# Kernel tuning notes

Hardware: AMD Instinct MI355X
Metric: run time of the kernel (lower is better)

The kernel has to match this reference:

```python
import jax, jax.numpy as jnp
import numpy as np

D_MODEL = 1024
N_HEADS = 16
D_FF = 2 * D_MODEL
EPS = 1e-6


def setup_inputs() -> dict:
    key = jax.random.key(0)
    ks = jax.random.split(key, 12)
    B, S, D = 2, 2048, D_MODEL
    w = lambda k, shape: (jax.random.normal(k, shape, dtype=jnp.float32) * 0.02)
    return {
        "x": jax.random.normal(ks[0], (B, S, D), dtype=jnp.float32),
        "mask": jnp.ones((B, S, S), dtype=jnp.int32),
        "alpha1": jnp.ones((D,), jnp.float32),
        "bias1": jnp.zeros((D,), jnp.float32),
        "Wq": w(ks[1], (D, D)), "bq": jnp.zeros((D,), jnp.float32),
        "Wk": w(ks[2], (D, D)), "bk": jnp.zeros((D,), jnp.float32),
        "Wv": w(ks[3], (D, D)), "bv": jnp.zeros((D,), jnp.float32),
        "Wo": w(ks[4], (D, D)), "bo": jnp.zeros((D,), jnp.float32),
        "alpha2": jnp.ones((D,), jnp.float32),
        "bias2": jnp.zeros((D,), jnp.float32),
        "W1": w(ks[5], (D, D_FF)), "b1": jnp.zeros((D_FF,), jnp.float32),
        "W2": w(ks[6], (D_FF, D)), "b2": jnp.zeros((D,), jnp.float32),
    }


def _norm(x, alpha, bias):
    # torch: alpha*(x-mean)/(std+eps)+bias, std is unbiased (ddof=1)
    mu = jnp.mean(x, axis=-1, keepdims=True)
    sd = jnp.std(x, axis=-1, ddof=1, keepdims=True)
    return alpha * (x - mu) / (sd + EPS) + bias


def _gelu(x):
    return jax.nn.gelu(x, approximate=False)  # torch F.gelu exact


def _attention(x2, mask, Wq, bq, Wk, bk, Wv, bv, Wo, bo):
    B, S, D = x2.shape
    h, dk = N_HEADS, D // N_HEADS
    # project and split heads: [B, h, S, dk]
    q = (x2 @ Wq + bq).reshape(B, S, h, dk).transpose(0, 2, 1, 3)
    k = (x2 @ Wk + bk).reshape(B, S, h, dk).transpose(0, 2, 1, 3)
    v = (x2 @ Wv + bv).reshape(B, S, h, dk).transpose(0, 2, 1, 3)
    scores = jnp.einsum('bhqd,bhkd->bhqk', q, k) / np.sqrt(dk).astype(np.float32)
    scores = jnp.where(mask[:, None] == 0, jnp.float32(-1e9), scores)
    attn = jax.nn.softmax(scores, axis=-1)
    out = jnp.einsum('bhqk,bhkd->bhqd', attn, v)
    out = out.transpose(0, 2, 1, 3).reshape(B, S, D)
    return out @ Wo + bo


def reference(x, mask, alpha1, bias1, Wq, bq, Wk, bk, Wv, bv, Wo, bo,
              alpha2, bias2, W1, b1, W2, b2):
    x2 = _norm(x, alpha1, bias1)
    x = x + _attention(x2, mask, Wq, bq, Wk, bk, Wv, bv, Wo, bo)
    x2 = _norm(x, alpha2, bias2)
    ff = _gelu(_gelu(x2 @ W1 + b1) @ W2 + b2)
    return x + ff
```

## Files before the change

kernel.cpp:

```cpp
#include <hip/hip_runtime.h>
#include <math.h>

typedef __attribute__((ext_vector_type(8))) short v8s;
typedef __attribute__((ext_vector_type(4))) float v4f;
typedef __attribute__((ext_vector_type(16))) float v16f;
typedef __attribute__((ext_vector_type(4))) unsigned int v4u;
typedef __attribute__((ext_vector_type(2))) unsigned int v2u;

#define MFMA16(a,b,c) __builtin_amdgcn_mfma_f32_16x16x32_bf16(a,b,c,0,0,0)
#define MFMA32(a,b,c) __builtin_amdgcn_mfma_f32_32x32x16_bf16(a,b,c,0,0,0)
#define QSCALE 0.18033688011112042f

typedef const __attribute__((address_space(1))) void* gp1_t;
typedef __attribute__((address_space(3))) void* lp3_t;
__device__ __forceinline__ void gll16(const void* g, void* l){
  __builtin_amdgcn_global_load_lds((gp1_t)g, (lp3_t)l, 16, 0, 0);
}
#define VMCNT(n) asm volatile("s_waitcnt vmcnt(" #n ")" ::: "memory")

__device__ __forceinline__ unsigned short f2b(float f){
  unsigned u = __builtin_bit_cast(unsigned, f);
  u += 0x7FFFu + ((u>>16)&1u);
  return (unsigned short)(u>>16);
}
__device__ __forceinline__ unsigned cvtpk(float lo, float hi){
  unsigned r;
  asm("v_cvt_pk_bf16_f32 %0, %1, %2" : "=v"(r) : "v"(lo), "v"(hi));
  return r;
}
__device__ __forceinline__ float gelu_exact(float x){
  return 0.5f*x*(1.0f + erff(x*0.70710678118654752f));
}

__global__ __launch_bounds__(256) void ln_kernel(const float* __restrict__ x,
    const float* __restrict__ alpha, const float* __restrict__ bias,
    unsigned short* __restrict__ out)
{
  const int D = 1024;
  int row = blockIdx.x;
  int tid = threadIdx.x;
  const float* xr = x + (size_t)row*D;
  v4f v = ((const v4f*)xr)[tid];
  float s  = v[0]+v[1]+v[2]+v[3];
  float s2 = v[0]*v[0]+v[1]*v[1]+v[2]*v[2]+v[3]*v[3];
  #pragma unroll
  for (int off=1; off<64; off<<=1){ s += __shfl_xor(s, off); s2 += __shfl_xor(s2, off); }
  __shared__ float red[8];
  int w = tid>>6;
  if ((tid&63)==0){ red[w]=s; red[4+w]=s2; }
  __syncthreads();
  s  = red[0]+red[1]+red[2]+red[3];
  s2 = red[4]+red[5]+red[6]+red[7];
  float mu  = s*(1.0f/D);
  float var = (s2 - (float)D*mu*mu)*(1.0f/(D-1));
  float inv = 1.0f/(sqrtf(fmaxf(var,0.0f)) + 1e-6f);
  v4f a  = ((const v4f*)alpha)[tid];
  v4f bi = ((const v4f*)bias)[tid];
  unsigned short o[4];
  #pragma unroll
  for (int i=0;i<4;i++) o[i] = f2b(a[i]*(v[i]-mu)*inv + bi[i]);
  v2u pk; pk[0] = (unsigned)o[0] | ((unsigned)o[1]<<16);
          pk[1] = (unsigned)o[2] | ((unsigned)o[3]<<16);
  ((v2u*)(out + (size_t)row*D))[tid] = pk;
}

__global__ __launch_bounds__(256) void transpose_f2b(const float* __restrict__ in,
    unsigned short* __restrict__ out, int K, int N)
{
  __shared__ float t[32][33];
  int n0 = blockIdx.x*32, k0 = blockIdx.y*32;
  int tx = threadIdx.x, ty = threadIdx.y;
  #pragma unroll
  for (int j=0;j<4;j++) t[ty+8*j][tx] = in[(size_t)(k0+ty+8*j)*N + n0+tx];
  __syncthreads();
  #pragma unroll
  for (int j=0;j<4;j++) out[(size_t)(n0+ty+8*j)*K + k0+tx] = f2b(t[tx][ty+8*j]);
}

__global__ __launch_bounds__(256) void mask_flags(const int* __restrict__ mask,
    unsigned char* __restrict__ flags)
{
  const int S = 2048;
  int bid = blockIdx.x;
  int kt = bid & 31, qt = (bid>>5)&31, b = bid>>10;
  int tid = threadIdx.x;
  const int* mp = mask + (size_t)b*S*S + (size_t)(qt*64)*S + kt*64;
  int ok = 1;
  #pragma unroll
  for (int i=0;i<16;i++){
    int idx = tid + i*256;
    int row = idx>>6, col = idx&63;
    ok &= (mp[(size_t)row*S + col] != 0);
  }
  ok = __all(ok) ? 1 : 0;
  __shared__ int f[4];
  if ((tid&63)==0) f[tid>>6] = ok;
  __syncthreads();
  if (tid==0) flags[bid] = (unsigned char)(f[0]&f[1]&f[2]&f[3]);
}

__global__ __launch_bounds__(256) void v_transpose(const unsigned short* __restrict__ vB,
    unsigned short* __restrict__ vT)
{
  __shared__ unsigned short ts[64][68];
  int tt = blockIdx.x & 31, bh = blockIdx.x >> 5;
  int b = bh >> 4, h = bh & 15;
  int tid = threadIdx.x;
  int row = tid>>3, c8 = (tid&7)*8;
  const unsigned short* src = vB + ((size_t)(b*2048 + tt*64))*1024 + h*64;
  #pragma unroll
  for (int j=0;j<2;j++)
    *(v4u*)&ts[row+32*j][c8] = *(const v4u*)(src + (size_t)(row+32*j)*1024 + c8);
  __syncthreads();
  unsigned short* dst = vT + ((size_t)bh*64)*2048 + (size_t)tt*64;
  #pragma unroll
  for (int j=0;j<2;j++){
    int d = row + 32*j;
    unsigned short tmp[8];
    #pragma unroll
    for (int jj=0;jj<8;jj++) tmp[jj] = ts[c8+jj][d];
    *(v4u*)&dst[(size_t)d*2048 + c8] = *(const v4u*)tmp;
  }
}

__global__ __launch_bounds__(256) void gemm_qkv(
    const unsigned short* __restrict__ A, const unsigned short* __restrict__ Bt,
    const float* __restrict__ bq, const float* __restrict__ bk, const float* __restrict__ bv,
    unsigned short* __restrict__ qB, unsigned short* __restrict__ kB, unsigned short* __restrict__ vB)
{
  const int K = 1024, N = 1024;
  __shared__ unsigned short As[3][128][32];
  __shared__ unsigned short Bs[3][128][32];
  int m0 = blockIdx.x*128;
  int ny = blockIdx.y;
  int seg = ny>>3;
  int n0g = ny*128;
  int tid = threadIdx.x;
  int w = tid>>6, l = tid&63;
  int wm = (w>>1)*64, wn = (w&1)*64;
  int r16 = l&15, kq = l>>4;
  v4f acc[4][4] = {};
  int t4 = tid>>2, c8 = (tid&3)*8;
  const unsigned short* Ag = A  + (size_t)(m0 + t4)*K + c8;
  const unsigned short* Bg = Bt + (size_t)(n0g + t4)*K + c8;
  auto stageG = [&](int kb, int idx){
    char* a = (char*)&As[idx][0][0] + w*1024;
    char* b = (char*)&Bs[idx][0][0] + w*1024;
    gll16(Ag + kb,                a);
    gll16(Ag + (size_t)64*K + kb, a + 4096);
    gll16(Bg + kb,                b);
    gll16(Bg + (size_t)64*K + kb, b + 4096);
  };
  const int nk = K/32;
  stageG(0, 0); stageG(32, 1);
  for (int i=0; i<nk; i++){
    int cur = i%3;
    if (i+1 < nk) VMCNT(4); else VMCNT(0);
    __builtin_amdgcn_s_barrier();
    if (i+2 < nk) stageG((i+2)*32, (i+2)%3);
    v8s a[4], b[4];
    #pragma unroll
    for (int mi=0;mi<4;mi++) a[mi] = *(const v8s*)&As[cur][wm+mi*16+r16][kq*8];
    #pragma unroll
    for (int ni=0;ni<4;ni++) b[ni] = *(const v8s*)&Bs[cur][wn+ni*16+r16][kq*8];
    #pragma unroll
    for (int mi=0;mi<4;mi++)
      #pragma unroll
      for (int ni=0;ni<4;ni++)
        acc[mi][ni] = MFMA16(a[mi], b[ni], acc[mi][ni]);
  }
  unsigned short* ob = (seg==0) ? qB : (seg==1) ? kB : vB;
  const float*    bp = (seg==0) ? bq : (seg==1) ? bk : bv;
  float sc = (seg==0) ? QSCALE : 1.0f;
  int ncol0 = (ny&7)*128;
  #pragma unroll
  for (int mi=0;mi<4;mi++){
    #pragma unroll
    for (int ni=0;ni<4;ni++){
      int col = ncol0 + wn + ni*16 + r16;
      float bvv = bp[col];
      #pragma unroll
      for (int r=0;r<4;r++){
        int row = m0 + wm + mi*16 + kq*4 + r;
        ob[(size_t)row*N + col] = f2b((acc[mi][ni][r] + bvv)*sc);
      }
    }
  }
}

template<int MODE>
__global__ __launch_bounds__(256) void gemm_bt(
    const unsigned short* __restrict__ A, const unsigned short* __restrict__ Bt,
    const float* __restrict__ bias, const float* __restrict__ res,
    unsigned short* __restrict__ outb, float* __restrict__ outf,
    int M, int N, int K)
{
  __shared__ unsigned short As[3][128][32];
  __shared__ unsigned short Bs[3][128][32];
  int m0 = blockIdx.x*128, n0 = blockIdx.y*128;
  int tid = threadIdx.x;
  int w = tid>>6, l = tid&63;
  int wm = (w>>1)*64, wn = (w&1)*64;
  int r16 = l&15, kq = l>>4;
  v4f acc[4][4] = {};
  int t4 = tid>>2, c8 = (tid&3)*8;
  const unsigned short* Ag = A  + (size_t)(m0 + t4)*K + c8;
  const unsigned short* Bg = Bt + (size_t)(n0 + t4)*K + c8;
  auto stageG = [&](int kb, int idx){
    char* a = (char*)&As[idx][0][0] + w*1024;
    char* b = (char*)&Bs[idx][0][0] + w*1024;
    gll16(Ag + kb,                a);
    gll16(Ag + (size_t)64*K + kb, a + 4096);
    gll16(Bg + kb,                b);
    gll16(Bg + (size_t)64*K + kb, b + 4096);
  };
  const int nk = K/32;
  stageG(0, 0); stageG(32, 1);
  for (int i=0; i<nk; i++){
    int cur = i%3;
    if (i+1 < nk) VMCNT(4); else VMCNT(0);
    __builtin_amdgcn_s_barrier();
    if (i+2 < nk) stageG((i+2)*32, (i+2)%3);
    v8s a[4], b[4];
    #pragma unroll
    for (int mi=0;mi<4;mi++) a[mi] = *(const v8s*)&As[cur][wm+mi*16+r16][kq*8];
    #pragma unroll
    for (int ni=0;ni<4;ni++) b[ni] = *(const v8s*)&Bs[cur][wn+ni*16+r16][kq*8];
    #pragma unroll
    for (int mi=0;mi<4;mi++)
      #pragma unroll
      for (int ni=0;ni<4;ni++)
        acc[mi][ni] = MFMA16(a[mi], b[ni], acc[mi][ni]);
  }
  #pragma unroll
  for (int mi=0;mi<4;mi++){
    #pragma unroll
    for (int ni=0;ni<4;ni++){
      int col = n0 + wn + ni*16 + r16;
      float bv = bias[col];
      #pragma unroll
      for (int r=0;r<4;r++){
        int row = m0 + wm + mi*16 + kq*4 + r;
        float t = acc[mi][ni][r] + bv;
        if (MODE==2) t = gelu_exact(t);
        if (MODE==2) outb[(size_t)row*N + col] = f2b(t);
        else         outf[(size_t)row*N + col] = t + res[(size_t)row*N + col];
      }
    }
  }
}

template<int MODE>
__global__ __launch_bounds__(256) void gemm64_bt(
    const unsigned short* __restrict__ A, const unsigned short* __restrict__ Bt,
    const float* __restrict__ bias, const float* __restrict__ res,
    float* __restrict__ outf, int M, int N, int K)
{
  __shared__ unsigned short As[3][64][32];
  __shared__ unsigned short Bs[3][128][32];
  int m0 = blockIdx.x*64, n0 = blockIdx.y*128;
  int tid = threadIdx.x;
  int w = tid>>6, l = tid&63;
  int wm = (w>>1)*32, wn = (w&1)*64;
  int r16 = l&15, kq = l>>4;
  v4f acc[2][4] = {};
  int t4 = tid>>2, c8 = (tid&3)*8;
  const unsigned short* Ag = A  + (size_t)(m0 + t4)*K + c8;
  const unsigned short* Bg = Bt + (size_t)(n0 + t4)*K + c8;
  auto stageG = [&](int kb, int idx){
    char* a = (char*)&As[idx][0][0] + w*1024;
    char* b = (char*)&Bs[idx][0][0] + w*1024;
    gll16(Ag + kb,                a);
    gll16(Bg + kb,                b);
    gll16(Bg + (size_t)64*K + kb, b + 4096);
  };
  const int nk = K/32;
  stageG(0, 0); stageG(32, 1);
  for (int i=0; i<nk; i++){
    int cur = i%3;
    if (i+1 < nk) VMCNT(3); else VMCNT(0);
    __builtin_amdgcn_s_barrier();
    if (i+2 < nk) stageG((i+2)*32, (i+2)%3);
    v8s a[2], b[4];
    #pragma unroll
    for (int mi=0;mi<2;mi++) a[mi] = *(const v8s*)&As[cur][wm+mi*16+r16][kq*8];
    #pragma unroll
    for (int ni=0;ni<4;ni++) b[ni] = *(const v8s*)&Bs[cur][wn+ni*16+r16][kq*8];
    #pragma unroll
    for (int mi=0;mi<2;mi++)
      #pragma unroll
      for (int ni=0;ni<4;ni++)
        acc[mi][ni] = MFMA16(a[mi], b[ni], acc[mi][ni]);
  }
  #pragma unroll
  for (int mi=0;mi<2;mi++){
    #pragma unroll
    for (int ni=0;ni<4;ni++){
      int col = n0 + wn + ni*16 + r16;
      float bv = bias[col];
      #pragma unroll
      for (int r=0;r<4;r++){
        int row = m0 + wm + mi*16 + kq*4 + r;
        float t = acc[mi][ni][r] + bv;
        if (MODE==3) t = gelu_exact(t);
        outf[(size_t)row*N + col] = t + res[(size_t)row*N + col];
      }
    }
  }
}

__global__ __launch_bounds__(256, 3) void attn_kernel(
    const unsigned short* __restrict__ Q, const unsigned short* __restrict__ Kb,
    const unsigned short* __restrict__ vT, const int* __restrict__ mask,
    const unsigned char* __restrict__ flags, unsigned short* __restrict__ out)
{
  const int S = 2048, D = 1024;
  __shared__ unsigned short Kb3[3][64][64];
  __shared__ unsigned short Vb3[3][64][64];
  int bid = (blockIdx.x & 7)*64 + (blockIdx.x >> 3);
  int qt = bid & 15;
  int bh = bid >> 4;
  int b = bh >> 4, h = bh & 15;
  int tid = threadIdx.x, w = tid>>6, l = tid&63;
  int l31 = l & 31, hi = l >> 5;
  int pidx = (l ^ 32) << 2;
  const unsigned short* Qp  = Q  + (size_t)b*S*D + h*64;
  const unsigned short* Kp  = Kb + (size_t)b*S*D + h*64;
  const unsigned short* vTp = vT + (size_t)bh*64*S;
  int qrow0 = qt*128 + w*32;
  int qrow  = qrow0 + l31;
  v8s qfr[4];
  #pragma unroll
  for (int ks=0;ks<4;ks++)
    qfr[ks] = *(const v8s*)(Qp + (size_t)qrow*D + ks*16 + hi*8);
  float m_run = -1e30f, l_run = 0.0f;
  v16f o0 = {}, o1 = {};
  const int* mp = mask + (size_t)b*S*S;
  const unsigned char* fl = flags + ((size_t)b*32 + qt*2)*32;
  unsigned long long okmask = __ballot( l < 32 ? ((fl[l] & fl[32+l]) != 0) : 1 );

  int srow = l>>3;
  int gsw  = (l&7) ^ srow;
  auto stage = [&](int kt, int idx){
    int kt64 = kt*64;
    #pragma unroll
    for (int sub=0; sub<2; sub++){
      int row = w*16 + sub*8 + srow;
      gll16(Kp  + (size_t)(kt64+row)*D + gsw*8, &Kb3[idx][w*16+sub*8][0]);
      gll16(vTp + (size_t)row*S + kt64 + gsw*8, &Vb3[idx][w*16+sub*8][0]);
    }
  };
  auto bfrag = [&](unsigned a0, unsigned a1, unsigned a4, unsigned a5) -> v8s {
    unsigned p0 = (unsigned)__builtin_amdgcn_ds_bpermute(pidx, (int)a0);
    unsigned p1 = (unsigned)__builtin_amdgcn_ds_bpermute(pidx, (int)a1);
    unsigned p4 = (unsigned)__builtin_amdgcn_ds_bpermute(pidx, (int)a4);
    unsigned p5 = (unsigned)__builtin_amdgcn_ds_bpermute(pidx, (int)a5);
    v4u pw;
    pw[0] = hi ? p4 : a0;
    pw[1] = hi ? p5 : a1;
    pw[2] = hi ? a4 : p0;
    pw[3] = hi ? a5 : p1;
    return __builtin_bit_cast(v8s, pw);
  };

  stage(0, 0); stage(1, 1);
  for (int kt=0; kt<32; kt++){
    int cur = kt%3;
    if (kt+1 < 32) VMCNT(4); else VMCNT(0);
    __builtin_amdgcn_s_barrier();
    if (kt+2 < 32) stage(kt+2, (kt+2)%3);
    int l7 = l & 7;
    v16f s0 = {}, s1 = {};
    __builtin_amdgcn_s_setprio(1);
    #pragma unroll
    for (int ks=0; ks<4; ks++){
      v8s kf0 = *(const v8s*)&Kb3[cur][l31     ][(((ks*2) + hi) ^ l7)*8];
      v8s kf1 = *(const v8s*)&Kb3[cur][32 + l31][(((ks*2) + hi) ^ l7)*8];
      s0 = MFMA32(kf0, qfr[ks], s0);
      s1 = MFMA32(kf1, qfr[ks], s1);
    }
    __builtin_amdgcn_s_setprio(0);
    if (((~okmask) >> kt) & 1ull){
      #pragma unroll
      for (int r=0;r<16;r++){
        int kvl = (r&3) + 8*(r>>2) + 4*hi;
        if (mp[(size_t)qrow*S + kt*64 + kvl]      == 0) s0[r] = -3.0e38f;
        if (mp[(size_t)qrow*S + kt*64 + 32 + kvl] == 0) s1[r] = -3.0e38f;
      }
    }
    float t0 = fmaxf(fmaxf(fmaxf(s0[0],s0[1]),fmaxf(s0[2],s0[3])),
                     fmaxf(fmaxf(s0[4],s0[5]),fmaxf(s0[6],s0[7])));
    float t1 = fmaxf(fmaxf(fmaxf(s0[8],s0[9]),fmaxf(s0[10],s0[11])),
                     fmaxf(fmaxf(s0[12],s0[13]),fmaxf(s0[14],s0[15])));
    float t2 = fmaxf(fmaxf(fmaxf(s1[0],s1[1]),fmaxf(s1[2],s1[3])),
                     fmaxf(fmaxf(s1[4],s1[5]),fmaxf(s1[6],s1[7])));
    float t3 = fmaxf(fmaxf(fmaxf(s1[8],s1[9]),fmaxf(s1[10],s1[11])),
                     fmaxf(fmaxf(s1[12],s1[13]),fmaxf(s1[14],s1[15])));
    float tm = fmaxf(fmaxf(t0,t1), fmaxf(t2,t3));
    tm = fmaxf(tm, __shfl_xor(tm, 32));
    if (!__all(tm <= m_run + 11.5f)){
      float mn = fmaxf(m_run, tm);
      float corr = exp2f(m_run - mn);
      m_run = mn;
      l_run *= corr;
      #pragma unroll
      for (int r=0;r<16;r++){ o0[r] *= corr; o1[r] *= corr; }
    }
    #pragma unroll
    for (int r=0;r<16;r++){
      s0[r] = exp2f(s0[r] - m_run);
      s1[r] = exp2f(s1[r] - m_run);
    }
    float a0 = ((s0[0]+s0[1])+(s0[2]+s0[3])) + ((s0[4]+s0[5])+(s0[6]+s0[7]));
    float a1 = ((s0[8]+s0[9])+(s0[10]+s0[11])) + ((s0[12]+s0[13])+(s0[14]+s0[15]));
    float a2 = ((s1[0]+s1[1])+(s1[2]+s1[3])) + ((s1[4]+s1[5])+(s1[6]+s1[7]));
    float a3 = ((s1[8]+s1[9])+(s1[10]+s1[11])) + ((s1[12]+s1[13])+(s1[14]+s1[15]));
    float rs = (a0+a1) + (a2+a3);
    rs += __shfl_xor(rs, 32);
    l_run += rs;
    v8s pb0 = bfrag(cvtpk(s0[0],s0[1]),  cvtpk(s0[2],s0[3]),
                    cvtpk(s0[4],s0[5]),  cvtpk(s0[6],s0[7]));
    v8s pb1 = bfrag(cvtpk(s0[8],s0[9]),  cvtpk(s0[10],s0[11]),
                    cvtpk(s0[12],s0[13]),cvtpk(s0[14],s0[15]));
    v8s pb2 = bfrag(cvtpk(s1[0],s1[1]),  cvtpk(s1[2],s1[3]),
                    cvtpk(s1[4],s1[5]),  cvtpk(s1[6],s1[7]));
    v8s pb3 = bfrag(cvtpk(s1[8],s1[9]),  cvtpk(s1[10],s1[11]),
                    cvtpk(s1[12],s1[13]),cvtpk(s1[14],s1[15]));
    __builtin_amdgcn_s_setprio(1);
    #pragma unroll
    for (int kvs=0; kvs<4; kvs++){
      v8s pb = (kvs==0) ? pb0 : (kvs==1) ? pb1 : (kvs==2) ? pb2 : pb3;
      v8s vv0 = *(const v8s*)&Vb3[cur][l31     ][(((kvs*2) + hi) ^ l7)*8];
      v8s vv1 = *(const v8s*)&Vb3[cur][32 + l31][(((kvs*2) + hi) ^ l7)*8];
      o0 = MFMA32(vv0, pb, o0);
      o1 = MFMA32(vv1, pb, o1);
    }
    __builtin_amdgcn_s_setprio(0);
  }
  float invl = 1.0f / l_run;
  size_t obase = (size_t)(b*S + qrow)*D + h*64;
  #pragma unroll
  for (int p=0; p<8; p++){
    int dk = (p&1)*2 + 8*(p>>1) + 4*hi;
    *(unsigned*)(out + obase + dk)      = cvtpk(o0[2*p]*invl, o0[2*p+1]*invl);
    *(unsigned*)(out + obase + 32 + dk) = cvtpk(o1[2*p]*invl, o1[2*p+1]*invl);
  }
}

extern "C" void kernel_launch(void* const* d_in, const int* in_sizes, int n_in,
                              void* d_out, int out_size, void* d_ws, size_t ws_size,
                              hipStream_t stream)
{
  const int D=1024, DFF=2048, BS=4096;
  const float* x      = (const float*)d_in[0];
  const int*   mask   = (const int*)d_in[1];
  const float* alpha1 = (const float*)d_in[2];
  const float* bias1  = (const float*)d_in[3];
  const float* Wq     = (const float*)d_in[4];
  const float* bq     = (const float*)d_in[5];
  const float* Wk     = (const float*)d_in[6];
  const float* bk     = (const float*)d_in[7];
  const float* Wv     = (const float*)d_in[8];
  const float* bv     = (const float*)d_in[9];
  const float* Wo     = (const float*)d_in[10];
  const float* bo     = (const float*)d_in[11];
  const float* alpha2 = (const float*)d_in[12];
  const float* bias2  = (const float*)d_in[13];
  const float* W1     = (const float*)d_in[14];
  const float* b1     = (const float*)d_in[15];
  const float* W2     = (const float*)d_in[16];
  const float* b2     = (const float*)d_in[17];
  float* outp = (float*)d_out;

  char* ws = (char*)d_ws;
  size_t off = 0;
  auto alloc = [&](size_t bytes){ void* p = ws+off; off += (bytes+255)&~(size_t)255; return p; };
  unsigned short* x2b    = (unsigned short*)alloc((size_t)BS*D*2);
  unsigned short* qB     = (unsigned short*)alloc((size_t)BS*D*2);
  unsigned short* kB     = (unsigned short*)alloc((size_t)BS*D*2);
  unsigned short* vB     = (unsigned short*)alloc((size_t)BS*D*2);
  unsigned short* attnB  = (unsigned short*)alloc((size_t)BS*D*2);
  unsigned short* h1     = (unsigned short*)alloc((size_t)BS*DFF*2);
  float*          xres   = (float*)alloc((size_t)BS*D*4);
  unsigned short* wqkvT  = (unsigned short*)alloc((size_t)3*D*D*2);
  unsigned short* woT    = (unsigned short*)alloc((size_t)D*D*2);
  unsigned short* w1T    = (unsigned short*)alloc((size_t)D*DFF*2);
  unsigned short* w2T    = (unsigned short*)alloc((size_t)DFF*D*2);
  unsigned char*  flg    = (unsigned char*)alloc(2048);
  unsigned short* vTb    = x2b;

  dim3 tb(32,8);
  transpose_f2b<<<dim3(D/32,  D/32 ), tb, 0, stream>>>(Wq, wqkvT,           D, D);
  transpose_f2b<<<dim3(D/32,  D/32 ), tb, 0, stream>>>(Wk, wqkvT + D*D,     D, D);
  transpose_f2b<<<dim3(D/32,  D/32 ), tb, 0, stream>>>(Wv, wqkvT + 2*D*D,   D, D);
  transpose_f2b<<<dim3(D/32,  D/32 ), tb, 0, stream>>>(Wo, woT, D, D);
  transpose_f2b<<<dim3(DFF/32,D/32 ), tb, 0, stream>>>(W1, w1T, D, DFF);
  transpose_f2b<<<dim3(D/32,  DFF/32), tb, 0, stream>>>(W2, w2T, DFF, D);

  mask_flags<<<2048, 256, 0, stream>>>(mask, flg);
  ln_kernel<<<BS, 256, 0, stream>>>(x, alpha1, bias1, x2b);

  gemm_qkv<<<dim3(BS/128, 24), 256, 0, stream>>>(x2b, wqkvT, bq, bk, bv, qB, kB, vB);

  v_transpose<<<1024, 256, 0, stream>>>(vB, vTb);

  attn_kernel<<<512, 256, 0, stream>>>(qB, kB, vTb, mask, flg, attnB);

  gemm64_bt<1><<<dim3(BS/64, D/128), 256, 0, stream>>>(attnB, woT, bo, x, xres, BS, D, D);

  ln_kernel<<<BS, 256, 0, stream>>>(xres, alpha2, bias2, x2b);

  gemm_bt<2><<<dim3(BS/128, DFF/128), 256, 0, stream>>>(x2b, w1T, b1, nullptr, h1, nullptr, BS, DFF, D);
  gemm64_bt<3><<<dim3(BS/64, D/128), 256, 0, stream>>>(h1, w2T, b2, xres, outp, BS, D, DFF);
}
```

Before: 262.3 us.

## Split attention KV range in two halves and merge partials in combine kernel

Splits each attention block's key/value sequence into two halves (flash-decoding style split-K), doubling the grid to 1024 blocks. Each half writes unnormalized fp32 partial outputs plus running max and sum, and a new combine kernel rescales and merges them into bf16. The KV staging drops from triple to double buffering with __syncthreads, and the occupancy hint rises to 4 blocks. The aim is to fill more CUs with only 512 blocks available. The cost is an extra kernel launch and roughly 32 MB of fp32 partial traffic.

```diff
diff --git a/kernel.cpp b/kernel.cpp
--- a/kernel.cpp
+++ b/kernel.cpp
@@ -3,6 +3,7 @@
 
 typedef __attribute__((ext_vector_type(8))) short v8s;
 typedef __attribute__((ext_vector_type(4))) float v4f;
+typedef __attribute__((ext_vector_type(2))) float v2f;
 typedef __attribute__((ext_vector_type(16))) float v16f;
 typedef __attribute__((ext_vector_type(4))) unsigned int v4u;
 typedef __attribute__((ext_vector_type(2))) unsigned int v2u;
@@ -309,17 +310,19 @@
   }
 }
 
-__global__ __launch_bounds__(256, 3) void attn_kernel(
+__global__ __launch_bounds__(256, 4) void attn_kernel(
     const unsigned short* __restrict__ Q, const unsigned short* __restrict__ Kb,
     const unsigned short* __restrict__ vT, const int* __restrict__ mask,
-    const unsigned char* __restrict__ flags, unsigned short* __restrict__ out)
+    const unsigned char* __restrict__ flags,
+    float* __restrict__ Opart, float* __restrict__ ml)
 {
   const int S = 2048, D = 1024;
-  __shared__ unsigned short Kb3[3][64][64];
-  __shared__ unsigned short Vb3[3][64][64];
-  int bid = (blockIdx.x & 7)*64 + (blockIdx.x >> 3);
-  int qt = bid & 15;
-  int bh = bid >> 4;
+  __shared__ unsigned short Kb2[2][64][64];
+  __shared__ unsigned short Vb2[2][64][64];
+  int bid = (blockIdx.x & 7)*128 + (blockIdx.x >> 3);
+  int half = bid & 1;
+  int qt = (bid >> 1) & 15;
+  int bh = bid >> 5;
   int b = bh >> 4, h = bh & 15;
   int tid = threadIdx.x, w = tid>>6, l = tid&63;
   int l31 = l & 31, hi = l >> 5;
@@ -327,8 +330,7 @@
   const unsigned short* Qp  = Q  + (size_t)b*S*D + h*64;
   const unsigned short* Kp  = Kb + (size_t)b*S*D + h*64;
   const unsigned short* vTp = vT + (size_t)bh*64*S;
-  int qrow0 = qt*128 + w*32;
-  int qrow  = qrow0 + l31;
+  int qrow = qt*128 + w*32 + l31;
   v8s qfr[4];
   #pragma unroll
   for (int ks=0;ks<4;ks++)
@@ -337,17 +339,18 @@
   v16f o0 = {}, o1 = {};
   const int* mp = mask + (size_t)b*S*S;
   const unsigned char* fl = flags + ((size_t)b*32 + qt*2)*32;
-  unsigned long long okmask = __ballot( l < 32 ? ((fl[l] & fl[32+l]) != 0) : 1 );
+  int kt0 = half*16;
+  unsigned long long okmask = __ballot( l < 16 ? ((fl[kt0+l] & fl[32+kt0+l]) != 0) : 1 );
 
   int srow = l>>3;
   int gsw  = (l&7) ^ srow;
-  auto stage = [&](int kt, int idx){
-    int kt64 = kt*64;
+  auto stage = [&](int ktg, int idx){
+    int kt64 = ktg*64;
     #pragma unroll
     for (int sub=0; sub<2; sub++){
       int row = w*16 + sub*8 + srow;
-      gll16(Kp  + (size_t)(kt64+row)*D + gsw*8, &Kb3[idx][w*16+sub*8][0]);
-      gll16(vTp + (size_t)row*S + kt64 + gsw*8, &Vb3[idx][w*16+sub*8][0]);
+      gll16(Kp  + (size_t)(kt64+row)*D + gsw*8, &Kb2[idx][w*16+sub*8][0]);
+      gll16(vTp + (size_t)row*S + kt64 + gsw*8, &Vb2[idx][w*16+sub*8][0]);
     }
   };
   auto bfrag = [&](unsigned a0, unsigned a1, unsigned a4, unsigned a5) -> v8s {
@@ -363,29 +366,29 @@
     return __builtin_bit_cast(v8s, pw);
   };
 
-  stage(0, 0); stage(1, 1);
-  for (int kt=0; kt<32; kt++){
-    int cur = kt%3;
-    if (kt+1 < 32) VMCNT(4); else VMCNT(0);
-    __builtin_amdgcn_s_barrier();
-    if (kt+2 < 32) stage(kt+2, (kt+2)%3);
+  stage(kt0, 0);
+  int cur = 0;
+  for (int it=0; it<16; it++){
+    __syncthreads();
+    if (it+1 < 16) stage(kt0+it+1, cur^1);
+    int ktg = kt0 + it;
     int l7 = l & 7;
     v16f s0 = {}, s1 = {};
     __builtin_amdgcn_s_setprio(1);
     #pragma unroll
     for (int ks=0; ks<4; ks++){
-      v8s kf0 = *(const v8s*)&Kb3[cur][l31     ][(((ks*2) + hi) ^ l7)*8];
-      v8s kf1 = *(const v8s*)&Kb3[cur][32 + l31][(((ks*2) + hi) ^ l7)*8];
+      v8s kf0 = *(const v8s*)&Kb2[cur][l31     ][(((ks*2) + hi) ^ l7)*8];
+      v8s kf1 = *(const v8s*)&Kb2[cur][32 + l31][(((ks*2) + hi) ^ l7)*8];
       s0 = MFMA32(kf0, qfr[ks], s0);
       s1 = MFMA32(kf1, qfr[ks], s1);
     }
     __builtin_amdgcn_s_setprio(0);
-    if (((~okmask) >> kt) & 1ull){
+    if (((~okmask) >> it) & 1ull){
       #pragma unroll
       for (int r=0;r<16;r++){
         int kvl = (r&3) + 8*(r>>2) + 4*hi;
-        if (mp[(size_t)qrow*S + kt*64 + kvl]      == 0) s0[r] = -3.0e38f;
-        if (mp[(size_t)qrow*S + kt*64 + 32 + kvl] == 0) s1[r] = -3.0e38f;
+        if (mp[(size_t)qrow*S + ktg*64 + kvl]      == 0) s0[r] = -3.0e38f;
+        if (mp[(size_t)qrow*S + ktg*64 + 32 + kvl] == 0) s1[r] = -3.0e38f;
       }
     }
     float t0 = fmaxf(fmaxf(fmaxf(s0[0],s0[1]),fmaxf(s0[2],s0[3])),
@@ -430,21 +433,51 @@
     #pragma unroll
     for (int kvs=0; kvs<4; kvs++){
       v8s pb = (kvs==0) ? pb0 : (kvs==1) ? pb1 : (kvs==2) ? pb2 : pb3;
-      v8s vv0 = *(const v8s*)&Vb3[cur][l31     ][(((kvs*2) + hi) ^ l7)*8];
-      v8s vv1 = *(const v8s*)&Vb3[cur][32 + l31][(((kvs*2) + hi) ^ l7)*8];
+      v8s vv0 = *(const v8s*)&Vb2[cur][l31     ][(((kvs*2) + hi) ^ l7)*8];
+      v8s vv1 = *(const v8s*)&Vb2[cur][32 + l31][(((kvs*2) + hi) ^ l7)*8];
       o0 = MFMA32(vv0, pb, o0);
       o1 = MFMA32(vv1, pb, o1);
     }
     __builtin_amdgcn_s_setprio(0);
-  }
-  float invl = 1.0f / l_run;
-  size_t obase = (size_t)(b*S + qrow)*D + h*64;
+    cur ^= 1;
+  }
+  int rowg = b*S + qrow;
+  float* Op = Opart + (size_t)half*4096*1024 + (size_t)rowg*1024 + h*64;
   #pragma unroll
   for (int p=0; p<8; p++){
     int dk = (p&1)*2 + 8*(p>>1) + 4*hi;
-    *(unsigned*)(out + obase + dk)      = cvtpk(o0[2*p]*invl, o0[2*p+1]*invl);
-    *(unsigned*)(out + obase + 32 + dk) = cvtpk(o1[2*p]*invl, o1[2*p+1]*invl);
-  }
+    v2f w0; w0[0] = o0[2*p]; w0[1] = o0[2*p+1];
+    v2f w1; w1[0] = o1[2*p]; w1[1] = o1[2*p+1];
+    *(v2f*)(Op + dk)      = w0;
+    *(v2f*)(Op + 32 + dk) = w1;
+  }
+  if (!hi){
+    float* mlp = ml + ((size_t)half*4096 + rowg)*32 + h*2;
+    mlp[0] = m_run;
+    mlp[1] = l_run;
+  }
+}
+
+__global__ __launch_bounds__(256) void attn_combine(const float* __restrict__ Opart,
+    const float* __restrict__ ml, unsigned short* __restrict__ outB)
+{
+  int row = blockIdx.x;
+  int t = threadIdx.x;
+  int col = t*4;
+  int head = col >> 6;
+  const float* m1p = ml + (size_t)row*32 + head*2;
+  const float* m2p = ml + ((size_t)4096 + row)*32 + head*2;
+  float m1 = m1p[0], l1 = m1p[1];
+  float m2 = m2p[0], l2 = m2p[1];
+  float M = fmaxf(m1, m2);
+  float w1 = exp2f(m1 - M), w2 = exp2f(m2 - M);
+  float inv = 1.0f / (l1*w1 + l2*w2);
+  v4f a = *(const v4f*)(Opart + (size_t)row*1024 + col);
+  v4f b = *(const v4f*)(Opart + (size_t)4096*1024 + (size_t)row*1024 + col);
+  v2u pk;
+  pk[0] = cvtpk((a[0]*w1 + b[0]*w2)*inv, (a[1]*w1 + b[1]*w2)*inv);
+  pk[1] = cvtpk((a[2]*w1 + b[2]*w2)*inv, (a[3]*w1 + b[3]*w2)*inv);
+  *(v2u*)(outB + (size_t)row*1024 + col) = pk;
 }
 
 extern "C" void kernel_launch(void* const* d_in, const int* in_sizes, int n_in,
@@ -487,6 +520,8 @@
   unsigned short* w1T    = (unsigned short*)alloc((size_t)D*DFF*2);
   unsigned short* w2T    = (unsigned short*)alloc((size_t)DFF*D*2);
   unsigned char*  flg    = (unsigned char*)alloc(2048);
+  float*          Opart  = (float*)alloc((size_t)2*BS*D*4);
+  float*          mlbuf  = (float*)alloc((size_t)2*BS*16*2*4);
   unsigned short* vTb    = x2b;
 
   dim3 tb(32,8);
@@ -504,7 +539,8 @@
 
   v_transpose<<<1024, 256, 0, stream>>>(vB, vTb);
 
-  attn_kernel<<<512, 256, 0, stream>>>(qB, kB, vTb, mask, flg, attnB);
+  attn_kernel<<<1024, 256, 0, stream>>>(qB, kB, vTb, mask, flg, Opart, mlbuf);
+  attn_combine<<<4096, 256, 0, stream>>>(Opart, mlbuf, attnB);
 
   gemm64_bt<1><<<dim3(BS/64, D/128), 256, 0, stream>>>(attnB, woT, bo, x, xres, BS, D, D);
 
```

Measured after the change: 259.5 us. No clear change (-1.1%).
